# Kernel optimization log

Measured on AMD Instinct MI355X. Metric: run time of the kernel, lower is better.

## Reference

```python
import jax, jax.numpy as jnp
import numpy as np

B, S, IN, E, H, NL = 64, 512, 1024, 128, 8, 4
D = E // H  # head dim = 16


def setup_inputs() -> dict:
    key = jax.random.key(0)
    ks = jax.random.split(key, 12)
    rn = lambda k, shape: jax.random.normal(k, shape, jnp.float32) * 0.02
    x = jax.random.normal(ks[0], (B, S, IN), jnp.float32)
    # per-recording valid lengths; recording 0 full-length so no attention key row is all-masked
    lengths = jax.random.randint(ks[1], (B,), 1, S + 1).at[0].set(S)
    key_padding_mask = jnp.arange(S)[None, :] >= lengths[:, None]  # (B,S) True = pad
    return {
        'x': x,
        'key_padding_mask': key_padding_mask,
        'embed_w': rn(ks[2], (IN, E)), 'embed_b': jnp.zeros((E,), jnp.float32),
        'qkv_w': rn(ks[3], (NL, 3, E, E)), 'qkv_b': jnp.zeros((NL, 3, E), jnp.float32),
        'out_w': rn(ks[4], (NL, E, E)), 'out_b': jnp.zeros((NL, E), jnp.float32),
        'ln_g': jnp.ones((NL, E), jnp.float32), 'ln_b': jnp.zeros((NL, E), jnp.float32),
        'ff1_w': rn(ks[5], (NL, E, 4 * E)), 'ff1_b': jnp.zeros((NL, 4 * E), jnp.float32),
        'ff2_w': rn(ks[6], (NL, 4 * E, E)), 'ff2_b': jnp.zeros((NL, E), jnp.float32),
        'fc1_w': rn(ks[7], (E, 32)), 'fc1_b': jnp.zeros((32,), jnp.float32),
        'fc2_w': rn(ks[8], (32, 1)), 'fc2_b': jnp.zeros((1,), jnp.float32),
    }


def _ln(x, g, b):
    m = x.mean(-1, keepdims=True)
    v = x.var(-1, keepdims=True)
    return (x - m) / jnp.sqrt(v + 1e-5) * g + b


def _pos_enc(s, e):
    pos = jnp.arange(s, dtype=jnp.float32)[:, None]
    i = jnp.arange(e)[None, :]
    angle = pos / jnp.power(jnp.float32(10000.0), (2 * (i // 2)).astype(jnp.float32) / e)
    return jnp.where(i % 2 == 0, jnp.sin(angle), jnp.cos(angle))  # (S,E)


def reference(x, key_padding_mask, embed_w, embed_b, qkv_w, qkv_b, out_w, out_b,
              ln_g, ln_b, ff1_w, ff1_b, ff2_w, ff2_b, fc1_w, fc1_b, fc2_w, fc2_b):
    h = x @ embed_w + embed_b  # (B,S,E)
    pe = _pos_enc(S, E)
    scale = 1.0 / jnp.sqrt(jnp.float32(D))
    # module uses batch_first=False MHA on (B,S,E): attention runs across recordings.
    # key_padding_mask.T -> (S,B): masked keys are recordings, per epoch position.
    keymask = key_padding_mask.T[:, None, None, :]  # (S,1,1,B)
    for l in range(NL):
        h = h + pe[None]  # pos enc re-added every block (as in source)
        res = h
        q = (h @ qkv_w[l, 0] + qkv_b[l, 0]).reshape(B, S, H, D)
        k = (h @ qkv_w[l, 1] + qkv_b[l, 1]).reshape(B, S, H, D)
        v = (h @ qkv_w[l, 2] + qkv_b[l, 2]).reshape(B, S, H, D)
        scores = jnp.einsum('ishd,jshd->shij', q, k) * scale  # (S,H,B,B)
        scores = jnp.where(keymask, -jnp.inf, scores)
        attn = jax.nn.softmax(scores, axis=-1)
        o = jnp.einsum('shij,jshd->ishd', attn, v).reshape(B, S, E)
        o = o @ out_w[l] + out_b[l]
        h = _ln(o + res, ln_g[l], ln_b[l])
        res = h
        ffo = jax.nn.relu(h @ ff1_w[l] + ff1_b[l]) @ ff2_w[l] + ff2_b[l]
        h = _ln(ffo + res, ln_g[l], ln_b[l])  # same LN params reused, as in source
    # masked mean pool over epochs (vectorized replacement of the python loop)
    valid = (~key_padding_mask).astype(h.dtype)  # (B,S)
    mean = jnp.einsum('bse,bs->be', h, valid) / valid.sum(axis=1)[:, None]
    out = jax.nn.relu(mean @ fc1_w + fc1_b) @ fc2_w + fc2_b  # (B,1)
    return jax.nn.sigmoid(out)
```

## Files before the change

### kernel.cpp

```cpp
#include <hip/hip_runtime.h>

#define Bb 64
#define Ss 512
#define INn 1024
#define Ee 128
#define Hh 8
#define Dd 16
#define NLl 4

typedef unsigned short u16;
typedef __attribute__((ext_vector_type(8))) short short8;
typedef __attribute__((ext_vector_type(4))) float f32x4;

__device__ __forceinline__ float b2f(unsigned u) { return __uint_as_float(u << 16); }
__device__ __forceinline__ u16 f2b(float f) {
    unsigned u = __float_as_uint(f);
    unsigned r = u + 0x7FFFu + ((u >> 16) & 1u);
    return (u16)(r >> 16);
}
__device__ __forceinline__ uint2 pk4(float4 f) {
    uint2 r;
    r.x = (unsigned)f2b(f.x) | ((unsigned)f2b(f.y) << 16);
    r.y = (unsigned)f2b(f.z) | ((unsigned)f2b(f.w) << 16);
    return r;
}

#define GLOAD_LDS16(g, l) __builtin_amdgcn_global_load_lds( \
    (const __attribute__((address_space(1))) void*)(g),     \
    (__attribute__((address_space(3))) void*)(l), 16, 0, 0)

__global__ __launch_bounds__(256) void prep_kernel(const unsigned char* __restrict__ m,
                                                   int* __restrict__ lengths,
                                                   float* __restrict__ pe,
                                                   const float* __restrict__ ew,
                                                   const float* __restrict__ qw,
                                                   const float* __restrict__ ow,
                                                   const float* __restrict__ f1w,
                                                   const float* __restrict__ f2w,
                                                   u16* __restrict__ we, u16* __restrict__ wq,
                                                   u16* __restrict__ wo, u16* __restrict__ wf1,
                                                   u16* __restrict__ wf2) {
    const int bid = blockIdx.x, tid = threadIdx.x;
    if (bid == 0) {
        __shared__ int lf[3];
        __shared__ int part[256];
        if (tid < 3) lf[tid] = 0;
        __syncthreads();
        int l0 = 0, l1 = 0, l23 = 0;
        for (int i = tid * 128; i < tid * 128 + 128; ++i) {
            if (m[i]) { int md = i & 3; if (md == 0) l0 = 1; else if (md == 1) l1 = 1; else l23 = 1; }
        }
        if (l0) atomicOr(&lf[0], 1);
        if (l1) atomicOr(&lf[1], 1);
        if (l23) atomicOr(&lf[2], 1);
        __syncthreads();
        int enc = lf[1] ? 1 : (lf[2] ? 2 : 0);
        int b = tid >> 2, q = tid & 3, cnt = 0;
        for (int s = q * 128; s < q * 128 + 128; ++s) {
            int idx = b * Ss + s;
            int mm;
            if (enc == 1)      mm = (m[idx] != 0);
            else if (enc == 2) mm = (((const float*)(const void*)m)[idx] != 0.0f);
            else               mm = (((const int*)(const void*)m)[idx] != 0);
            cnt += (mm == 0);
        }
        part[tid] = cnt;
        __syncthreads();
        if (tid < 64)
            lengths[tid] = part[tid * 4] + part[tid * 4 + 1] + part[tid * 4 + 2] + part[tid * 4 + 3];
        return;
    }
    if (bid <= 2) {
        for (int i = tid; i < 32768; i += 256) {
            int idx = (bid - 1) * 32768 + i;
            int s = idx >> 7, e = idx & 127;
            float expo = (float)(2 * (e >> 1)) * (1.0f / 128.0f);
            float freq = powf(10000.0f, -expo);
            float angle = (float)s * freq;
            pe[idx] = (e & 1) ? cosf(angle) : sinf(angle);
        }
        return;
    }
    int tb = bid - 3;
    const float* src; u16* dst; int K, N, tile;
    if (tb < 32)       { src = ew;  dst = we;  K = 1024; N = 128; tile = tb; }
    else if (tb < 80)  { int b = tb - 32;  int mat = b >> 2; src = qw  + (size_t)mat * 16384; dst = wq  + (size_t)mat * 16384; K = 128; N = 128; tile = b & 3; }
    else if (tb < 96)  { int b = tb - 80;  int mat = b >> 2; src = ow  + (size_t)mat * 16384; dst = wo  + (size_t)mat * 16384; K = 128; N = 128; tile = b & 3; }
    else if (tb < 160) { int b = tb - 96;  int mat = b >> 4; src = f1w + (size_t)mat * 65536; dst = wf1 + (size_t)mat * 65536; K = 128; N = 512; tile = b & 15; }
    else               { int b = tb - 160; int mat = b >> 4; src = f2w + (size_t)mat * 65536; dst = wf2 + (size_t)mat * 65536; K = 512; N = 128; tile = b & 15; }
    int ktiles = K >> 6;
    int k0 = (tile % ktiles) * 64, n0 = (tile / ktiles) * 64;
    __shared__ __align__(16) u16 t_s[64 * 68];
    int r = tid >> 2, cq = (tid & 3) * 16;
    const float* sp = src + (size_t)(k0 + r) * N + n0 + cq;
#pragma unroll
    for (int i = 0; i < 4; ++i) {
        float4 f = *(const float4*)(sp + 4 * i);
        *(uint2*)&t_s[r * 68 + cq + 4 * i] = pk4(f);
    }
    __syncthreads();
    u16 tmp[16];
#pragma unroll
    for (int kk = 0; kk < 16; ++kk) tmp[kk] = t_s[(cq + kk) * 68 + r];
    int rowg = n0 + r;
    int x = (rowg & 7) << 3;
    u16* base = dst + (size_t)rowg * K;
    *(uint4*)(base + ((k0 + cq) ^ x))     = ((uint4*)tmp)[0];
    *(uint4*)(base + ((k0 + cq + 8) ^ x)) = ((uint4*)tmp)[1];
}

__global__ __launch_bounds__(256) void embed_gemm(const float* __restrict__ X,
                                                  const u16* __restrict__ Wt,
                                                  const float* __restrict__ bias,
                                                  const float* __restrict__ pe,
                                                  u16* __restrict__ C) {
    __shared__ __align__(16) u16 Af[64 * 68];
    __shared__ __align__(16) u16 Bs[128 * 64];
    const int tid = threadIdx.x;
    const int w = tid >> 6, lane = tid & 63, l16 = lane & 15, lhi = lane >> 4;
    const int row0 = blockIdx.x * 64;
    const int xr = (l16 & 7) << 3;
    f32x4 acc[8];
#pragma unroll
    for (int ni = 0; ni < 8; ++ni) acc[ni] = (f32x4){0.f, 0.f, 0.f, 0.f};

    const int ar = tid >> 2, ak = (tid & 3) * 16;
    const int crow = tid >> 3, cc8 = (tid & 7) * 8;
    const int wave_lds = w * 512;
    const u16* Bbase = Wt + cc8;
    const float* Arow = X + (size_t)(row0 + ar) * 1024 + ak;

    for (int k0 = 0; k0 < 1024; k0 += 64) {
        __syncthreads();
#pragma unroll
        for (int i = 0; i < 4; ++i)
            GLOAD_LDS16(Bbase + (size_t)(i * 32 + crow) * 1024 + k0, &Bs[i * 2048 + wave_lds]);
#pragma unroll
        for (int i = 0; i < 4; ++i) {
            float4 f = *(const float4*)(Arow + k0 + 4 * i);
            *(uint2*)&Af[ar * 68 + ak + 4 * i] = pk4(f);
        }
        __syncthreads();
#pragma unroll
        for (int ks = 0; ks < 2; ++ks) {
            short8 af;
            ((uint2*)&af)[0] = *(const uint2*)&Af[(w * 16 + l16) * 68 + ks * 32 + lhi * 8];
            ((uint2*)&af)[1] = *(const uint2*)&Af[(w * 16 + l16) * 68 + ks * 32 + lhi * 8 + 4];
#pragma unroll
            for (int ni = 0; ni < 8; ++ni) {
                short8 bfr = *(const short8*)&Bs[(ni * 16 + l16) * 64 + ((ks * 32 + lhi * 8) ^ xr)];
                acc[ni] = __builtin_amdgcn_mfma_f32_16x16x32_bf16(af, bfr, acc[ni], 0, 0, 0);
            }
        }
    }
    float biasr[8];
#pragma unroll
    for (int ni = 0; ni < 8; ++ni) biasr[ni] = bias[ni * 16 + l16];
#pragma unroll
    for (int reg = 0; reg < 4; ++reg) {
        int r = row0 + w * 16 + lhi * 4 + reg;
        int s = r & 511;
        int bidx = r >> 9;
        int orow = s * 64 + bidx;
        int xo = (bidx & 7) << 3;
        const float* per = pe + (size_t)s * 128;
        u16* crw = C + (size_t)orow * 128;
#pragma unroll
        for (int ni = 0; ni < 8; ++ni) {
            int c = ni * 16 + l16;
            crw[c ^ xo] = f2b(acc[ni][reg] + biasr[ni] + per[c]);
        }
    }
}

__global__ __launch_bounds__(256) void qkv_gemm(const u16* __restrict__ A,
                                                const u16* __restrict__ Wt,
                                                const float* __restrict__ bias,
                                                u16* __restrict__ Cq,
                                                u16* __restrict__ Ckv) {
    __shared__ __align__(16) u16 As[128 * 128];
    __shared__ __align__(16) u16 Bs[128 * 128];
    const int tid = threadIdx.x, w = tid >> 6, lane = tid & 63;
    const int l16 = lane & 15, lhi = lane >> 4;
    const int row0 = blockIdx.x * 128, col0 = blockIdx.y * 128;
    const int so = w * 512 + lane * 8;
    const int xr = (l16 & 7) << 3;
#pragma unroll
    for (int i = 0; i < 8; ++i) {
        GLOAD_LDS16(A + (size_t)row0 * 128 + i * 2048 + so, &As[i * 2048 + w * 512]);
        GLOAD_LDS16(Wt + (size_t)col0 * 128 + i * 2048 + so, &Bs[i * 2048 + w * 512]);
    }
    __syncthreads();
    f32x4 acc[2][8];
#pragma unroll
    for (int mi = 0; mi < 2; ++mi)
#pragma unroll
        for (int ni = 0; ni < 8; ++ni) acc[mi][ni] = (f32x4){0.f, 0.f, 0.f, 0.f};
#pragma unroll
    for (int ks = 0; ks < 4; ++ks) {
        const int ko = (ks * 32 + lhi * 8) ^ xr;
        short8 af[2], bfr[8];
#pragma unroll
        for (int mi = 0; mi < 2; ++mi)
            af[mi] = *(const short8*)&As[(w * 32 + mi * 16 + l16) * 128 + ko];
#pragma unroll
        for (int ni = 0; ni < 8; ++ni)
            bfr[ni] = *(const short8*)&Bs[(ni * 16 + l16) * 128 + ko];
#pragma unroll
        for (int mi = 0; mi < 2; ++mi)
#pragma unroll
            for (int ni = 0; ni < 8; ++ni)
                acc[mi][ni] = __builtin_amdgcn_mfma_f32_16x16x32_bf16(af[mi], bfr[ni], acc[mi][ni], 0, 0, 0);
    }
    float biasr[8];
#pragma unroll
    for (int ni = 0; ni < 8; ++ni) biasr[ni] = bias[col0 + ni * 16 + l16];
#pragma unroll
    for (int mi = 0; mi < 2; ++mi)
#pragma unroll
        for (int reg = 0; reg < 4; ++reg) {
            int r = row0 + w * 32 + mi * 16 + lhi * 4 + reg;
            u16* crw; int cbase;
            if (col0 == 0) { crw = Cq + (size_t)r * 128; cbase = 0; }
            else           { crw = Ckv + (size_t)r * 256; cbase = col0 - 128; }
#pragma unroll
            for (int ni = 0; ni < 8; ++ni)
                crw[cbase + ni * 16 + l16] = f2b(acc[mi][ni][reg] + biasr[ni]);
        }
}

__global__ __launch_bounds__(256) void attnout_kernel(const u16* __restrict__ qb,
                                                      const u16* __restrict__ kvb,
                                                      const u16* __restrict__ wo,
                                                      const float* __restrict__ outb,
                                                      const int* __restrict__ lengths,
                                                      const float* __restrict__ gamma,
                                                      const float* __restrict__ beta,
                                                      u16* __restrict__ h) {
    const int s = blockIdx.x;
    const int tid = threadIdx.x, w = tid >> 6, lane = tid & 63;
    const int l16 = lane & 15, lhi = lane >> 4;
    __shared__ __align__(16) u16 Vt[8 * 16 * 72];
    __shared__ __align__(16) u16 Ps[4 * 64 * 72];
    __shared__ __align__(16) u16 o_s[64 * 136];
    __shared__ int len_s[64];

    {
        int j = tid >> 2, c = tid & 3;
        const u16* src = kvb + ((size_t)(s * 64 + j)) * 256 + 128 + c * 32;
        u16 tmp[32];
        ((uint4*)tmp)[0] = *(const uint4*)src;
        ((uint4*)tmp)[1] = *(const uint4*)(src + 8);
        ((uint4*)tmp)[2] = *(const uint4*)(src + 16);
        ((uint4*)tmp)[3] = *(const uint4*)(src + 24);
#pragma unroll
        for (int e = 0; e < 32; ++e) {
            int hh = 2 * c + (e >> 4), d = e & 15;
            Vt[hh * 1152 + d * 72 + j] = tmp[e];
        }
    }
    if (tid < 64) len_s[tid] = lengths[tid];
    __syncthreads();

    bool mk[4];
#pragma unroll
    for (int jt = 0; jt < 4; ++jt) mk[jt] = (s >= len_s[jt * 16 + l16]);

    u16* pw = Ps + w * 4608;
#pragma unroll
    for (int hp = 0; hp < 2; ++hp) {
        const int hh = w * 2 + hp;
        short8 af[4];
#pragma unroll
        for (int it = 0; it < 4; ++it) {
            af[it] = (short8){0, 0, 0, 0, 0, 0, 0, 0};
            if (lhi < 2)
                af[it] = *(const short8*)(qb + ((size_t)(s * 64 + it * 16 + l16)) * 128 + hh * 16 + lhi * 8);
        }
        f32x4 sf[4][4];
#pragma unroll
        for (int jt = 0; jt < 4; ++jt) {
            short8 bf = (short8){0, 0, 0, 0, 0, 0, 0, 0};
            if (lhi < 2)
                bf = *(const short8*)(kvb + ((size_t)(s * 64 + jt * 16 + l16)) * 256 + hh * 16 + lhi * 8);
#pragma unroll
            for (int it = 0; it < 4; ++it)
                sf[it][jt] = __builtin_amdgcn_mfma_f32_16x16x32_bf16(af[it], bf, (f32x4){0.f, 0.f, 0.f, 0.f}, 0, 0, 0);
        }
        float inv[4][4];
#pragma unroll
        for (int it = 0; it < 4; ++it) {
#pragma unroll
            for (int reg = 0; reg < 4; ++reg) {
                float vv[4], mx = -1e30f;
#pragma unroll
                for (int jt = 0; jt < 4; ++jt) {
                    float xv = mk[jt] ? -1e30f : sf[it][jt][reg] * 0.25f;
                    vv[jt] = xv; mx = fmaxf(mx, xv);
                }
                mx = fmaxf(mx, __shfl_xor(mx, 1)); mx = fmaxf(mx, __shfl_xor(mx, 2));
                mx = fmaxf(mx, __shfl_xor(mx, 4)); mx = fmaxf(mx, __shfl_xor(mx, 8));
                float e4[4], sum = 0.f;
#pragma unroll
                for (int jt = 0; jt < 4; ++jt) {
                    float e = mk[jt] ? 0.f : __expf(vv[jt] - mx);
                    e4[jt] = e; sum += e;
                }
                sum += __shfl_xor(sum, 1); sum += __shfl_xor(sum, 2);
                sum += __shfl_xor(sum, 4); sum += __shfl_xor(sum, 8);
                inv[it][reg] = 1.0f / sum;
                int prow = it * 16 + lhi * 4 + reg;
#pragma unroll
                for (int jt = 0; jt < 4; ++jt)
                    pw[prow * 72 + jt * 16 + l16] = f2b(e4[jt]);
            }
        }
        f32x4 ao[4];
#pragma unroll
        for (int it = 0; it < 4; ++it) ao[it] = (f32x4){0.f, 0.f, 0.f, 0.f};
        short8 vb[2];
#pragma unroll
        for (int ksv = 0; ksv < 2; ++ksv)
            vb[ksv] = *(const short8*)&Vt[hh * 1152 + l16 * 72 + ksv * 32 + lhi * 8];
#pragma unroll
        for (int it = 0; it < 4; ++it)
#pragma unroll
            for (int ksv = 0; ksv < 2; ++ksv) {
                short8 pa = *(const short8*)&pw[(it * 16 + l16) * 72 + ksv * 32 + lhi * 8];
                ao[it] = __builtin_amdgcn_mfma_f32_16x16x32_bf16(pa, vb[ksv], ao[it], 0, 0, 0);
            }
#pragma unroll
        for (int it = 0; it < 4; ++it)
#pragma unroll
            for (int reg = 0; reg < 4; ++reg)
                o_s[(it * 16 + lhi * 4 + reg) * 136 + hh * 16 + l16] = f2b(ao[it][reg] * inv[it][reg]);
    }
    __syncthreads();

    const int xr = (l16 & 7) << 3;
    f32x4 acc[8];
#pragma unroll
    for (int ni = 0; ni < 8; ++ni) acc[ni] = (f32x4){0.f, 0.f, 0.f, 0.f};
#pragma unroll
    for (int ks = 0; ks < 4; ++ks) {
        short8 af = *(const short8*)&o_s[(w * 16 + l16) * 136 + ks * 32 + lhi * 8];
#pragma unroll
        for (int ni = 0; ni < 8; ++ni) {
            short8 bf = *(const short8*)(wo + (size_t)(ni * 16 + l16) * 128 + ((ks * 32 + lhi * 8) ^ xr));
            acc[ni] = __builtin_amdgcn_mfma_f32_16x16x32_bf16(af, bf, acc[ni], 0, 0, 0);
        }
    }
    float biasr[8], gr[8], br[8];
#pragma unroll
    for (int ni = 0; ni < 8; ++ni) {
        int c = ni * 16 + l16;
        biasr[ni] = outb[c]; gr[ni] = gamma[c]; br[ni] = beta[c];
    }
#pragma unroll
    for (int reg = 0; reg < 4; ++reg) {
        int row = w * 16 + lhi * 4 + reg;
        int xo = (row & 7) << 3;
        size_t rbase = ((size_t)(s * 64 + row)) * 128;
        float v[8], sm = 0.f, s2 = 0.f;
#pragma unroll
        for (int ni = 0; ni < 8; ++ni) {
            float x = acc[ni][reg] + biasr[ni] + b2f(h[rbase + ((ni * 16 + l16) ^ xo)]);
            v[ni] = x; sm += x; s2 += x * x;
        }
        sm += __shfl_xor(sm, 1); sm += __shfl_xor(sm, 2);
        sm += __shfl_xor(sm, 4); sm += __shfl_xor(sm, 8);
        s2 += __shfl_xor(s2, 1); s2 += __shfl_xor(s2, 2);
        s2 += __shfl_xor(s2, 4); s2 += __shfl_xor(s2, 8);
        float mean = sm * (1.0f / 128.0f);
        float var = s2 * (1.0f / 128.0f) - mean * mean;
        float rstd = rsqrtf(fmaxf(var, 0.0f) + 1e-5f);
#pragma unroll
        for (int ni = 0; ni < 8; ++ni)
            h[rbase + ((ni * 16 + l16) ^ xo)] = f2b((v[ni] - mean) * rstd * gr[ni] + br[ni]);
    }
}

__global__ __launch_bounds__(256) void ff_fused(const u16* __restrict__ hbuf,
                                                const u16* __restrict__ w1t,
                                                const u16* __restrict__ w2t,
                                                const float* __restrict__ b1,
                                                const float* __restrict__ b2,
                                                const float* __restrict__ gamma,
                                                const float* __restrict__ beta,
                                                const float* __restrict__ pe,
                                                u16* __restrict__ hout) {
    __shared__ __align__(16) u16 A_s[16384];
    __shared__ __align__(16) u16 W1_s[16384];
    __shared__ __align__(16) u16 W2_s[16384];
    __shared__ __align__(16) u16 T_s[16384];
    const int tid = threadIdx.x, w = tid >> 6, lane = tid & 63;
    const int l16 = lane & 15, lhi = lane >> 4;
    const int row0 = blockIdx.x * 128;
    const int so = w * 512 + lane * 8;
    const int xr = (l16 & 7) << 3;
#pragma unroll
    for (int i = 0; i < 8; ++i)
        GLOAD_LDS16(hbuf + (size_t)row0 * 128 + i * 2048 + so, &A_s[i * 2048 + w * 512]);

    f32x4 acc2[2][8];
#pragma unroll
    for (int mi = 0; mi < 2; ++mi)
#pragma unroll
        for (int ni = 0; ni < 8; ++ni) acc2[mi][ni] = (f32x4){0.f, 0.f, 0.f, 0.f};

    for (int nc = 0; nc < 4; ++nc) {
        __syncthreads();
#pragma unroll
        for (int i = 0; i < 8; ++i) {
            GLOAD_LDS16(w1t + nc * 16384 + i * 2048 + so, &W1_s[i * 2048 + w * 512]);
            int slot = i * 2048 + so;
            GLOAD_LDS16(w2t + (size_t)(slot >> 7) * 512 + nc * 128 + (slot & 127),
                        &W2_s[i * 2048 + w * 512]);
        }
        __syncthreads();
        f32x4 acc1[2][8];
#pragma unroll
        for (int mi = 0; mi < 2; ++mi)
#pragma unroll
            for (int ni = 0; ni < 8; ++ni) acc1[mi][ni] = (f32x4){0.f, 0.f, 0.f, 0.f};
#pragma unroll
        for (int ks = 0; ks < 4; ++ks) {
            const int ko = (ks * 32 + lhi * 8) ^ xr;
            short8 af[2], bfr[8];
#pragma unroll
            for (int mi = 0; mi < 2; ++mi)
                af[mi] = *(const short8*)&A_s[(w * 32 + mi * 16 + l16) * 128 + ko];
#pragma unroll
            for (int ni = 0; ni < 8; ++ni)
                bfr[ni] = *(const short8*)&W1_s[(ni * 16 + l16) * 128 + ko];
#pragma unroll
            for (int mi = 0; mi < 2; ++mi)
#pragma unroll
                for (int ni = 0; ni < 8; ++ni)
                    acc1[mi][ni] = __builtin_amdgcn_mfma_f32_16x16x32_bf16(af[mi], bfr[ni], acc1[mi][ni], 0, 0, 0);
        }
        float bb[8];
#pragma unroll
        for (int ni = 0; ni < 8; ++ni) bb[ni] = b1[nc * 128 + ni * 16 + l16];
#pragma unroll
        for (int mi = 0; mi < 2; ++mi)
#pragma unroll
            for (int reg = 0; reg < 4; ++reg) {
                int xt = ((lhi * 4 + reg) & 7) << 3;
#pragma unroll
                for (int ni = 0; ni < 8; ++ni)
                    T_s[(w * 32 + mi * 16 + lhi * 4 + reg) * 128 + ((ni * 16 + l16) ^ xt)] =
                        f2b(fmaxf(acc1[mi][ni][reg] + bb[ni], 0.0f));
            }
#pragma unroll
        for (int ks = 0; ks < 4; ++ks) {
            const int ko = (ks * 32 + lhi * 8) ^ xr;
            short8 pa[2], bfr[8];
#pragma unroll
            for (int mi = 0; mi < 2; ++mi)
                pa[mi] = *(const short8*)&T_s[(w * 32 + mi * 16 + l16) * 128 + ko];
#pragma unroll
            for (int ni = 0; ni < 8; ++ni)
                bfr[ni] = *(const short8*)&W2_s[(ni * 16 + l16) * 128 + ko];
#pragma unroll
            for (int mi = 0; mi < 2; ++mi)
#pragma unroll
                for (int ni = 0; ni < 8; ++ni)
                    acc2[mi][ni] = __builtin_amdgcn_mfma_f32_16x16x32_bf16(pa[mi], bfr[ni], acc2[mi][ni], 0, 0, 0);
        }
    }
    float b2r[8], gr[8], br[8];
#pragma unroll
    for (int ni = 0; ni < 8; ++ni) {
        int c = ni * 16 + l16;
        b2r[ni] = b2[c]; gr[ni] = gamma[c]; br[ni] = beta[c];
    }
#pragma unroll
    for (int mi = 0; mi < 2; ++mi)
#pragma unroll
        for (int reg = 0; reg < 4; ++reg) {
            int lrow = w * 32 + mi * 16 + lhi * 4 + reg;
            int r = row0 + lrow;
            int xo = (lrow & 7) << 3;
            float v[8], sm = 0.f, s2 = 0.f;
#pragma unroll
            for (int ni = 0; ni < 8; ++ni) {
                float x = acc2[mi][ni][reg] + b2r[ni] + b2f(A_s[lrow * 128 + ((ni * 16 + l16) ^ xo)]);
                v[ni] = x; sm += x; s2 += x * x;
            }
            sm += __shfl_xor(sm, 1); sm += __shfl_xor(sm, 2);
            sm += __shfl_xor(sm, 4); sm += __shfl_xor(sm, 8);
            s2 += __shfl_xor(s2, 1); s2 += __shfl_xor(s2, 2);
            s2 += __shfl_xor(s2, 4); s2 += __shfl_xor(s2, 8);
            float mean = sm * (1.0f / 128.0f);
            float var = s2 * (1.0f / 128.0f) - mean * mean;
            float rstd = rsqrtf(fmaxf(var, 0.0f) + 1e-5f);
            u16* crw = hout + (size_t)r * 128;
#pragma unroll
            for (int ni = 0; ni < 8; ++ni) {
                int c = ni * 16 + l16;
                float val = (v[ni] - mean) * rstd * gr[ni] + br[ni];
                if (pe) val += pe[(size_t)(r >> 6) * 128 + c];
                crw[c ^ xo] = f2b(val);
            }
        }
}

__global__ __launch_bounds__(256) void poolhead_kernel(const u16* __restrict__ h,
                                                       const int* __restrict__ lengths,
                                                       const float* __restrict__ fc1w,
                                                       const float* __restrict__ fc1b,
                                                       const float* __restrict__ fc2w,
                                                       const float* __restrict__ fc2b,
                                                       float* __restrict__ out) {
    int b = blockIdx.x, tid = threadIdx.x;
    int e = tid & 127, half = tid >> 7;
    int len = lengths[b];
    int ep = e ^ ((b & 7) << 3);
    float s = 0.0f;
    for (int t = half; t < len; t += 2) s += b2f(h[((size_t)(t * 64 + b)) * 128 + ep]);
    __shared__ float red[256];
    __shared__ float mp[128];
    __shared__ float z[32];
    red[tid] = s;
    __syncthreads();
    if (tid < 128) mp[tid] = (red[tid] + red[tid + 128]) / (float)len;
    __syncthreads();
    if (tid < 32) {
        float a = fc1b[tid];
        for (int k = 0; k < 128; ++k) a = fmaf(mp[k], fc1w[k * 32 + tid], a);
        z[tid] = fmaxf(a, 0.0f);
    }
    __syncthreads();
    if (tid == 0) {
        float a = fc2b[0];
#pragma unroll
        for (int t = 0; t < 32; ++t) a = fmaf(z[t], fc2w[t], a);
        out[b] = 1.0f / (1.0f + expf(-a));
    }
}

extern "C" void kernel_launch(void* const* d_in, const int* in_sizes, int n_in,
                              void* d_out, int out_size, void* d_ws, size_t ws_size,
                              hipStream_t stream) {
    (void)in_sizes; (void)n_in; (void)out_size; (void)ws_size;
    const float* x        = (const float*)d_in[0];
    const unsigned char* mask = (const unsigned char*)d_in[1];
    const float* embed_w  = (const float*)d_in[2];
    const float* embed_b  = (const float*)d_in[3];
    const float* qkv_w    = (const float*)d_in[4];
    const float* qkv_b    = (const float*)d_in[5];
    const float* out_w    = (const float*)d_in[6];
    const float* out_b    = (const float*)d_in[7];
    const float* ln_g     = (const float*)d_in[8];
    const float* ln_b     = (const float*)d_in[9];
    const float* ff1_w    = (const float*)d_in[10];
    const float* ff1_b    = (const float*)d_in[11];
    const float* ff2_w    = (const float*)d_in[12];
    const float* ff2_b    = (const float*)d_in[13];
    const float* fc1_w    = (const float*)d_in[14];
    const float* fc1_b    = (const float*)d_in[15];
    const float* fc2_w    = (const float*)d_in[16];
    const float* fc2_b    = (const float*)d_in[17];

    char* wsb = (char*)d_ws;
    int*   lengths = (int*)wsb;
    float* pe      = (float*)(wsb + 512);
    u16* wt_embed  = (u16*)(wsb + 262656);
    u16* wt_qkv    = (u16*)(wsb + 524800);
    u16* wt_out    = (u16*)(wsb + 918016);
    u16* wt_ff1    = (u16*)(wsb + 1049088);
    u16* wt_ff2    = (u16*)(wsb + 1573376);
    u16* hbuf      = (u16*)(wsb + 2097664);
    u16* qb        = (u16*)(wsb + 10486272);
    u16* kvb       = (u16*)(wsb + 18874880);

    prep_kernel<<<227, 256, 0, stream>>>(mask, lengths, pe,
                                         embed_w, qkv_w, out_w, ff1_w, ff2_w,
                                         wt_embed, wt_qkv, wt_out, wt_ff1, wt_ff2);

    embed_gemm<<<512, 256, 0, stream>>>(x, wt_embed, embed_b, pe, hbuf);

    for (int l = 0; l < NLl; ++l) {
        qkv_gemm<<<dim3(256, 3), 256, 0, stream>>>(
            hbuf, wt_qkv + (size_t)l * 49152, qkv_b + l * 384, qb, kvb);
        attnout_kernel<<<512, 256, 0, stream>>>(
            qb, kvb, wt_out + (size_t)l * 16384, out_b + l * 128,
            lengths, ln_g + l * 128, ln_b + l * 128, hbuf);
        ff_fused<<<256, 256, 0, stream>>>(
            hbuf, wt_ff1 + (size_t)l * 65536, wt_ff2 + (size_t)l * 65536,
            ff1_b + l * 512, ff2_b + l * 128,
            ln_g + l * 128, ln_b + l * 128, (l < 3) ? pe : nullptr, hbuf);
    }

    poolhead_kernel<<<64, 256, 0, stream>>>(hbuf, lengths, fc1_w, fc1_b, fc2_w, fc2_b,
                                            (float*)d_out);
}
```

Before: 427.7 us.

## Restructure FF tiling, double-buffer embed weights, drop V transpose, spread PE prep

The fused feed-forward kernel now takes 64-row tiles (512 blocks) with 64-wide hidden chunks and smaller LDS buffers, which raises occupancy and prefetches the next W1/W2 chunks between barriers. The embed GEMM double-buffers its weight tiles so the next global-to-LDS load overlaps the MFMAs. Attention loads V directly from global with strided scalar reads instead of staging a transposed copy in LDS. Positional-encoding prep is spread over 32 blocks instead of 2. Costs include more barriers and weight reloads per row in the FF kernel, and uncoalesced 2-byte V reads.

After: 388.5 us. 1.1x faster.

```diff
diff --git a/kernel.cpp b/kernel.cpp
--- a/kernel.cpp
+++ b/kernel.cpp
@@ -28,6 +28,8 @@
 #define GLOAD_LDS16(g, l) __builtin_amdgcn_global_load_lds( \
     (const __attribute__((address_space(1))) void*)(g),     \
     (__attribute__((address_space(3))) void*)(l), 16, 0, 0)
+
+#define MFMA16(a, b, c) __builtin_amdgcn_mfma_f32_16x16x32_bf16((a), (b), (c), 0, 0, 0)
 
 __global__ __launch_bounds__(256) void prep_kernel(const unsigned char* __restrict__ m,
                                                    int* __restrict__ lengths,
@@ -70,9 +72,9 @@
             lengths[tid] = part[tid * 4] + part[tid * 4 + 1] + part[tid * 4 + 2] + part[tid * 4 + 3];
         return;
     }
-    if (bid <= 2) {
-        for (int i = tid; i < 32768; i += 256) {
-            int idx = (bid - 1) * 32768 + i;
+    if (bid <= 32) {
+        for (int i = tid; i < 2048; i += 256) {
+            int idx = (bid - 1) * 2048 + i;
             int s = idx >> 7, e = idx & 127;
             float expo = (float)(2 * (e >> 1)) * (1.0f / 128.0f);
             float freq = powf(10000.0f, -expo);
@@ -81,7 +83,7 @@
         }
         return;
     }
-    int tb = bid - 3;
+    int tb = bid - 33;
     const float* src; u16* dst; int K, N, tile;
     if (tb < 32)       { src = ew;  dst = we;  K = 1024; N = 128; tile = tb; }
     else if (tb < 80)  { int b = tb - 32;  int mat = b >> 2; src = qw  + (size_t)mat * 16384; dst = wq  + (size_t)mat * 16384; K = 128; N = 128; tile = b & 3; }
@@ -115,7 +117,7 @@
                                                   const float* __restrict__ pe,
                                                   u16* __restrict__ C) {
     __shared__ __align__(16) u16 Af[64 * 68];
-    __shared__ __align__(16) u16 Bs[128 * 64];
+    __shared__ __align__(16) u16 Bs[2][128 * 64];
     const int tid = threadIdx.x;
     const int w = tid >> 6, lane = tid & 63, l16 = lane & 15, lhi = lane >> 4;
     const int row0 = blockIdx.x * 64;
@@ -130,17 +132,25 @@
     const u16* Bbase = Wt + cc8;
     const float* Arow = X + (size_t)(row0 + ar) * 1024 + ak;
 
-    for (int k0 = 0; k0 < 1024; k0 += 64) {
-        __syncthreads();
-#pragma unroll
-        for (int i = 0; i < 4; ++i)
-            GLOAD_LDS16(Bbase + (size_t)(i * 32 + crow) * 1024 + k0, &Bs[i * 2048 + wave_lds]);
+#pragma unroll
+    for (int i = 0; i < 4; ++i)
+        GLOAD_LDS16(Bbase + (size_t)(i * 32 + crow) * 1024, &Bs[0][i * 2048 + wave_lds]);
+
+    for (int it = 0; it < 16; ++it) {
+        const int k0 = it * 64;
+        __syncthreads();
 #pragma unroll
         for (int i = 0; i < 4; ++i) {
             float4 f = *(const float4*)(Arow + k0 + 4 * i);
             *(uint2*)&Af[ar * 68 + ak + 4 * i] = pk4(f);
         }
         __syncthreads();
+        if (it < 15) {
+#pragma unroll
+            for (int i = 0; i < 4; ++i)
+                GLOAD_LDS16(Bbase + (size_t)(i * 32 + crow) * 1024 + k0 + 64,
+                            &Bs[(it + 1) & 1][i * 2048 + wave_lds]);
+        }
 #pragma unroll
         for (int ks = 0; ks < 2; ++ks) {
             short8 af;
@@ -148,8 +158,8 @@
             ((uint2*)&af)[1] = *(const uint2*)&Af[(w * 16 + l16) * 68 + ks * 32 + lhi * 8 + 4];
 #pragma unroll
             for (int ni = 0; ni < 8; ++ni) {
-                short8 bfr = *(const short8*)&Bs[(ni * 16 + l16) * 64 + ((ks * 32 + lhi * 8) ^ xr)];
-                acc[ni] = __builtin_amdgcn_mfma_f32_16x16x32_bf16(af, bfr, acc[ni], 0, 0, 0);
+                short8 bfr = *(const short8*)&Bs[it & 1][(ni * 16 + l16) * 64 + ((ks * 32 + lhi * 8) ^ xr)];
+                acc[ni] = MFMA16(af, bfr, acc[ni]);
             }
         }
     }
@@ -210,7 +220,7 @@
         for (int mi = 0; mi < 2; ++mi)
 #pragma unroll
             for (int ni = 0; ni < 8; ++ni)
-                acc[mi][ni] = __builtin_amdgcn_mfma_f32_16x16x32_bf16(af[mi], bfr[ni], acc[mi][ni], 0, 0, 0);
+                acc[mi][ni] = MFMA16(af[mi], bfr[ni], acc[mi][ni]);
     }
     float biasr[8];
 #pragma unroll
@@ -240,25 +250,10 @@
     const int s = blockIdx.x;
     const int tid = threadIdx.x, w = tid >> 6, lane = tid & 63;
     const int l16 = lane & 15, lhi = lane >> 4;
-    __shared__ __align__(16) u16 Vt[8 * 16 * 72];
     __shared__ __align__(16) u16 Ps[4 * 64 * 72];
     __shared__ __align__(16) u16 o_s[64 * 136];
     __shared__ int len_s[64];
 
-    {
-        int j = tid >> 2, c = tid & 3;
-        const u16* src = kvb + ((size_t)(s * 64 + j)) * 256 + 128 + c * 32;
-        u16 tmp[32];
-        ((uint4*)tmp)[0] = *(const uint4*)src;
-        ((uint4*)tmp)[1] = *(const uint4*)(src + 8);
-        ((uint4*)tmp)[2] = *(const uint4*)(src + 16);
-        ((uint4*)tmp)[3] = *(const uint4*)(src + 24);
-#pragma unroll
-        for (int e = 0; e < 32; ++e) {
-            int hh = 2 * c + (e >> 4), d = e & 15;
-            Vt[hh * 1152 + d * 72 + j] = tmp[e];
-        }
-    }
     if (tid < 64) len_s[tid] = lengths[tid];
     __syncthreads();
 
@@ -284,8 +279,10 @@
             if (lhi < 2)
                 bf = *(const short8*)(kvb + ((size_t)(s * 64 + jt * 16 + l16)) * 256 + hh * 16 + lhi * 8);
 #pragma unroll
-            for (int it = 0; it < 4; ++it)
-                sf[it][jt] = __builtin_amdgcn_mfma_f32_16x16x32_bf16(af[it], bf, (f32x4){0.f, 0.f, 0.f, 0.f}, 0, 0, 0);
+            for (int it = 0; it < 4; ++it) {
+                f32x4 z = {0.f, 0.f, 0.f, 0.f};
+                sf[it][jt] = MFMA16(af[it], bf, z);
+            }
         }
         float inv[4][4];
 #pragma unroll
@@ -321,13 +318,16 @@
         short8 vb[2];
 #pragma unroll
         for (int ksv = 0; ksv < 2; ++ksv)
-            vb[ksv] = *(const short8*)&Vt[hh * 1152 + l16 * 72 + ksv * 32 + lhi * 8];
+#pragma unroll
+            for (int e = 0; e < 8; ++e)
+                vb[ksv][e] = (short)kvb[((size_t)(s * 64 + ksv * 32 + lhi * 8 + e)) * 256
+                                        + 128 + hh * 16 + l16];
 #pragma unroll
         for (int it = 0; it < 4; ++it)
 #pragma unroll
             for (int ksv = 0; ksv < 2; ++ksv) {
                 short8 pa = *(const short8*)&pw[(it * 16 + l16) * 72 + ksv * 32 + lhi * 8];
-                ao[it] = __builtin_amdgcn_mfma_f32_16x16x32_bf16(pa, vb[ksv], ao[it], 0, 0, 0);
+                ao[it] = MFMA16(pa, vb[ksv], ao[it]);
             }
 #pragma unroll
         for (int it = 0; it < 4; ++it)
@@ -347,7 +347,7 @@
 #pragma unroll
         for (int ni = 0; ni < 8; ++ni) {
             short8 bf = *(const short8*)(wo + (size_t)(ni * 16 + l16) * 128 + ((ks * 32 + lhi * 8) ^ xr));
-            acc[ni] = __builtin_amdgcn_mfma_f32_16x16x32_bf16(af, bf, acc[ni], 0, 0, 0);
+            acc[ni] = MFMA16(af, bf, acc[ni]);
         }
     }
     float biasr[8], gr[8], br[8];
@@ -389,84 +389,87 @@
                                                 const float* __restrict__ beta,
                                                 const float* __restrict__ pe,
                                                 u16* __restrict__ hout) {
-    __shared__ __align__(16) u16 A_s[16384];
-    __shared__ __align__(16) u16 W1_s[16384];
-    __shared__ __align__(16) u16 W2_s[16384];
-    __shared__ __align__(16) u16 T_s[16384];
+    __shared__ __align__(16) u16 A_s[8192];
+    __shared__ __align__(16) u16 W1_s[8192];
+    __shared__ __align__(16) u16 W2_s[8192];
+    __shared__ __align__(16) u16 T_s[4096];
     const int tid = threadIdx.x, w = tid >> 6, lane = tid & 63;
     const int l16 = lane & 15, lhi = lane >> 4;
-    const int row0 = blockIdx.x * 128;
+    const int row0 = blockIdx.x * 64;
     const int so = w * 512 + lane * 8;
     const int xr = (l16 & 7) << 3;
-#pragma unroll
-    for (int i = 0; i < 8; ++i)
+
+#pragma unroll
+    for (int i = 0; i < 4; ++i)
         GLOAD_LDS16(hbuf + (size_t)row0 * 128 + i * 2048 + so, &A_s[i * 2048 + w * 512]);
-
-    f32x4 acc2[2][8];
-#pragma unroll
-    for (int mi = 0; mi < 2; ++mi)
-#pragma unroll
-        for (int ni = 0; ni < 8; ++ni) acc2[mi][ni] = (f32x4){0.f, 0.f, 0.f, 0.f};
-
-    for (int nc = 0; nc < 4; ++nc) {
-        __syncthreads();
-#pragma unroll
-        for (int i = 0; i < 8; ++i) {
-            GLOAD_LDS16(w1t + nc * 16384 + i * 2048 + so, &W1_s[i * 2048 + w * 512]);
-            int slot = i * 2048 + so;
-            GLOAD_LDS16(w2t + (size_t)(slot >> 7) * 512 + nc * 128 + (slot & 127),
-                        &W2_s[i * 2048 + w * 512]);
-        }
-        __syncthreads();
-        f32x4 acc1[2][8];
-#pragma unroll
-        for (int mi = 0; mi < 2; ++mi)
-#pragma unroll
-            for (int ni = 0; ni < 8; ++ni) acc1[mi][ni] = (f32x4){0.f, 0.f, 0.f, 0.f};
+#pragma unroll
+    for (int i = 0; i < 4; ++i) {
+        int slot = i * 2048 + so;
+        GLOAD_LDS16(w1t + (size_t)(slot >> 7) * 128 + ((slot & 127) ^ (((slot >> 7) & 7) << 3)),
+                    &W1_s[slot]);
+        GLOAD_LDS16(w2t + (size_t)(slot >> 6) * 512 + ((slot & 63) ^ (((slot >> 6) & 7) << 3)),
+                    &W2_s[slot]);
+    }
+    __syncthreads();
+
+    f32x4 acc2[8];
+#pragma unroll
+    for (int ni = 0; ni < 8; ++ni) acc2[ni] = (f32x4){0.f, 0.f, 0.f, 0.f};
+
+    for (int nc = 0; nc < 8; ++nc) {
+        f32x4 acc1[4];
+#pragma unroll
+        for (int ni = 0; ni < 4; ++ni) acc1[ni] = (f32x4){0.f, 0.f, 0.f, 0.f};
 #pragma unroll
         for (int ks = 0; ks < 4; ++ks) {
             const int ko = (ks * 32 + lhi * 8) ^ xr;
-            short8 af[2], bfr[8];
-#pragma unroll
-            for (int mi = 0; mi < 2; ++mi)
-                af[mi] = *(const short8*)&A_s[(w * 32 + mi * 16 + l16) * 128 + ko];
-#pragma unroll
-            for (int ni = 0; ni < 8; ++ni)
-                bfr[ni] = *(const short8*)&W1_s[(ni * 16 + l16) * 128 + ko];
-#pragma unroll
-            for (int mi = 0; mi < 2; ++mi)
-#pragma unroll
-                for (int ni = 0; ni < 8; ++ni)
-                    acc1[mi][ni] = __builtin_amdgcn_mfma_f32_16x16x32_bf16(af[mi], bfr[ni], acc1[mi][ni], 0, 0, 0);
-        }
-        float bb[8];
-#pragma unroll
-        for (int ni = 0; ni < 8; ++ni) bb[ni] = b1[nc * 128 + ni * 16 + l16];
-#pragma unroll
-        for (int mi = 0; mi < 2; ++mi)
-#pragma unroll
-            for (int reg = 0; reg < 4; ++reg) {
-                int xt = ((lhi * 4 + reg) & 7) << 3;
-#pragma unroll
-                for (int ni = 0; ni < 8; ++ni)
-                    T_s[(w * 32 + mi * 16 + lhi * 4 + reg) * 128 + ((ni * 16 + l16) ^ xt)] =
-                        f2b(fmaxf(acc1[mi][ni][reg] + bb[ni], 0.0f));
-            }
-#pragma unroll
-        for (int ks = 0; ks < 4; ++ks) {
+            short8 af = *(const short8*)&A_s[(w * 16 + l16) * 128 + ko];
+#pragma unroll
+            for (int ni = 0; ni < 4; ++ni) {
+                short8 bf = *(const short8*)&W1_s[(ni * 16 + l16) * 128 + ko];
+                acc1[ni] = MFMA16(af, bf, acc1[ni]);
+            }
+        }
+        float bb[4];
+#pragma unroll
+        for (int ni = 0; ni < 4; ++ni) bb[ni] = b1[nc * 64 + ni * 16 + l16];
+#pragma unroll
+        for (int reg = 0; reg < 4; ++reg) {
+            int xt = ((lhi * 4 + reg) & 7) << 3;
+#pragma unroll
+            for (int ni = 0; ni < 4; ++ni)
+                T_s[(w * 16 + lhi * 4 + reg) * 64 + ((ni * 16 + l16) ^ xt)] =
+                    f2b(fmaxf(acc1[ni][reg] + bb[ni], 0.0f));
+        }
+        __syncthreads();
+        if (nc < 7) {
+#pragma unroll
+            for (int i = 0; i < 4; ++i) {
+                int slot = i * 2048 + so;
+                GLOAD_LDS16(w1t + (size_t)((nc + 1) * 64 + (slot >> 7)) * 128
+                                + ((slot & 127) ^ (((slot >> 7) & 7) << 3)),
+                            &W1_s[slot]);
+            }
+        }
+#pragma unroll
+        for (int ks = 0; ks < 2; ++ks) {
             const int ko = (ks * 32 + lhi * 8) ^ xr;
-            short8 pa[2], bfr[8];
-#pragma unroll
-            for (int mi = 0; mi < 2; ++mi)
-                pa[mi] = *(const short8*)&T_s[(w * 32 + mi * 16 + l16) * 128 + ko];
-#pragma unroll
-            for (int ni = 0; ni < 8; ++ni)
-                bfr[ni] = *(const short8*)&W2_s[(ni * 16 + l16) * 128 + ko];
-#pragma unroll
-            for (int mi = 0; mi < 2; ++mi)
-#pragma unroll
-                for (int ni = 0; ni < 8; ++ni)
-                    acc2[mi][ni] = __builtin_amdgcn_mfma_f32_16x16x32_bf16(pa[mi], bfr[ni], acc2[mi][ni], 0, 0, 0);
+            short8 pa = *(const short8*)&T_s[(w * 16 + l16) * 64 + ko];
+#pragma unroll
+            for (int ni = 0; ni < 8; ++ni) {
+                short8 bf = *(const short8*)&W2_s[(ni * 16 + l16) * 64 + ko];
+                acc2[ni] = MFMA16(pa, bf, acc2[ni]);
+            }
+        }
+        __syncthreads();
+        if (nc < 7) {
+#pragma unroll
+            for (int i = 0; i < 4; ++i) {
+                int slot = i * 2048 + so;
+                GLOAD_LDS16(w2t + (size_t)(slot >> 6) * 512 + (nc + 1) * 64
+                                + ((slot & 63) ^ (((slot >> 6) & 7) << 3)),
+                            &W2_s[slot]);
+            }
         }
     }
     float b2r[8], gr[8], br[8];
@@ -476,34 +479,32 @@
         b2r[ni] = b2[c]; gr[ni] = gamma[c]; br[ni] = beta[c];
     }
 #pragma unroll
-    for (int mi = 0; mi < 2; ++mi)
-#pragma unroll
-        for (int reg = 0; reg < 4; ++reg) {
-            int lrow = w * 32 + mi * 16 + lhi * 4 + reg;
-            int r = row0 + lrow;
-            int xo = (lrow & 7) << 3;
-            float v[8], sm = 0.f, s2 = 0.f;
-#pragma unroll
-            for (int ni = 0; ni < 8; ++ni) {
-                float x = acc2[mi][ni][reg] + b2r[ni] + b2f(A_s[lrow * 128 + ((ni * 16 + l16) ^ xo)]);
-                v[ni] = x; sm += x; s2 += x * x;
-            }
-            sm += __shfl_xor(sm, 1); sm += __shfl_xor(sm, 2);
-            sm += __shfl_xor(sm, 4); sm += __shfl_xor(sm, 8);
-            s2 += __shfl_xor(s2, 1); s2 += __shfl_xor(s2, 2);
-            s2 += __shfl_xor(s2, 4); s2 += __shfl_xor(s2, 8);
-            float mean = sm * (1.0f / 128.0f);
-            float var = s2 * (1.0f / 128.0f) - mean * mean;
-            float rstd = rsqrtf(fmaxf(var, 0.0f) + 1e-5f);
-            u16* crw = hout + (size_t)r * 128;
-#pragma unroll
-            for (int ni = 0; ni < 8; ++ni) {
-                int c = ni * 16 + l16;
-                float val = (v[ni] - mean) * rstd * gr[ni] + br[ni];
-                if (pe) val += pe[(size_t)(r >> 6) * 128 + c];
-                crw[c ^ xo] = f2b(val);
-            }
-        }
+    for (int reg = 0; reg < 4; ++reg) {
+        int lrow = w * 16 + lhi * 4 + reg;
+        int r = row0 + lrow;
+        int xo = (lrow & 7) << 3;
+        float v[8], sm = 0.f, s2 = 0.f;
+#pragma unroll
+        for (int ni = 0; ni < 8; ++ni) {
+            float x = acc2[ni][reg] + b2r[ni] + b2f(A_s[lrow * 128 + ((ni * 16 + l16) ^ xo)]);
+            v[ni] = x; sm += x; s2 += x * x;
+        }
+        sm += __shfl_xor(sm, 1); sm += __shfl_xor(sm, 2);
+        sm += __shfl_xor(sm, 4); sm += __shfl_xor(sm, 8);
+        s2 += __shfl_xor(s2, 1); s2 += __shfl_xor(s2, 2);
+        s2 += __shfl_xor(s2, 4); s2 += __shfl_xor(s2, 8);
+        float mean = sm * (1.0f / 128.0f);
+        float var = s2 * (1.0f / 128.0f) - mean * mean;
+        float rstd = rsqrtf(fmaxf(var, 0.0f) + 1e-5f);
+        u16* crw = hout + (size_t)r * 128;
+#pragma unroll
+        for (int ni = 0; ni < 8; ++ni) {
+            int c = ni * 16 + l16;
+            float val = (v[ni] - mean) * rstd * gr[ni] + br[ni];
+            if (pe) val += pe[(size_t)(r >> 6) * 128 + c];
+            crw[c ^ xo] = f2b(val);
+        }
+    }
 }
 
 __global__ __launch_bounds__(256) void poolhead_kernel(const u16* __restrict__ h,
@@ -575,7 +576,7 @@
     u16* qb        = (u16*)(wsb + 10486272);
     u16* kvb       = (u16*)(wsb + 18874880);
 
-    prep_kernel<<<227, 256, 0, stream>>>(mask, lengths, pe,
+    prep_kernel<<<257, 256, 0, stream>>>(mask, lengths, pe,
                                          embed_w, qkv_w, out_w, ff1_w, ff2_w,
                                          wt_embed, wt_qkv, wt_out, wt_ff1, wt_ff2);
 
@@ -587,7 +588,7 @@
         attnout_kernel<<<512, 256, 0, stream>>>(
             qb, kvb, wt_out + (size_t)l * 16384, out_b + l * 128,
             lengths, ln_g + l * 128, ln_b + l * 128, hbuf);
-        ff_fused<<<256, 256, 0, stream>>>(
+        ff_fused<<<512, 256, 0, stream>>>(
             hbuf, wt_ff1 + (size_t)l * 65536, wt_ff2 + (size_t)l * 65536,
             ff1_b + l * 512, ff2_b + l * 128,
             ln_g + l * 128, ln_b + l * 128, (l < 3) ? pe : nullptr, hbuf);
```
